# Kernel tuning notes

Measured on AMD Instinct MI355X. Metric: run time of the kernel, lower is better.

Reference implementation:

```python
import jax, jax.numpy as jnp
import numpy as np

B, S, HID = 1, 2048, 2048
H, KV, D = 16, 8, 128          # heads, kv heads, head_dim
EPS = 1e-6
THETA_T, THETA_HW = 1000000.0, 10000.0
SCALE = D ** -0.5
NEG = -1e9


def _rms(x, w):
    xf = x.astype(jnp.float32)
    var = jnp.mean(xf * xf, axis=-1, keepdims=True)
    return (w * (xf * jax.lax.rsqrt(var + EPS))).astype(x.dtype)


def _rope_cs(pos, theta, half_dim):
    # Module builds RoPE with head_dim = 2*half_dim then takes every-other freq:
    # exponents arange(0, 2*half_dim, 4) / (2*half_dim)  -> half_dim//2 freqs
    dim2 = 2 * half_dim
    inv_freq = 1.0 / theta ** (jnp.arange(0, dim2, 4, dtype=jnp.float32) / dim2)
    freqs = pos.astype(jnp.float32)[:, None] * inv_freq[None, :]   # [S, half_dim//2]
    emb = jnp.concatenate([freqs, freqs], axis=-1)                 # [S, half_dim]
    return jnp.cos(emb), jnp.sin(emb)


def _rot_half(x):
    d = x.shape[-1] // 2
    return jnp.concatenate([-x[..., d:], x[..., :d]], axis=-1)


def _apply_rope(q, k, cos, sin):
    cos = cos[None, None]  # [1,1,S,dim]
    sin = sin[None, None]
    return q * cos + _rot_half(q) * sin, k * cos + _rot_half(k) * sin


def setup_inputs() -> dict:
    key = jax.random.key(0)
    ks = jax.random.split(key, 10)
    hidden_states = jax.random.normal(ks[0], (B, S, HID), jnp.float32)
    indexes = jax.random.randint(ks[1], (3, S), 0, S)
    causal = jnp.tril(jnp.ones((S, S), bool))
    attention_mask = jnp.where(causal, 0.0, NEG).astype(jnp.float32)[None, None]
    qkv_w = jax.random.normal(ks[2], ((H + 2 * KV) * D, HID), jnp.float32) * 0.02
    qkv_b = jax.random.normal(ks[3], ((H + 2 * KV) * D,), jnp.float32) * 0.02
    o_w = jax.random.normal(ks[4], (HID, H * D), jnp.float32) * 0.02
    o_b = jax.random.normal(ks[5], (HID,), jnp.float32) * 0.02
    q_norm_w = jnp.ones((D // 2,), jnp.float32)
    k_norm_w = jnp.ones((D // 2,), jnp.float32)
    q_norm_hw_w = jnp.ones((D // 2,), jnp.float32)
    k_norm_hw_w = jnp.ones((D // 2,), jnp.float32)
    return dict(hidden_states=hidden_states, indexes=indexes, attention_mask=attention_mask,
                qkv_w=qkv_w, qkv_b=qkv_b, o_w=o_w, o_b=o_b,
                q_norm_w=q_norm_w, k_norm_w=k_norm_w,
                q_norm_hw_w=q_norm_hw_w, k_norm_hw_w=k_norm_hw_w)


def reference(hidden_states, indexes, attention_mask, qkv_w, qkv_b, o_w, o_b,
              q_norm_w, k_norm_w, q_norm_hw_w, k_norm_hw_w):
    b, s, _ = hidden_states.shape
    qkv = hidden_states @ qkv_w.T + qkv_b
    q, k, v = jnp.split(qkv, [H * D, H * D + KV * D], axis=-1)
    q = q.reshape(b, s, H, D)
    k = k.reshape(b, s, KV, D)
    v = v.reshape(b, s, KV, D)

    # split head_dim into time half and hw half
    q_t, q_hw = jnp.split(q, 2, axis=-1)
    k_t, k_hw = jnp.split(k, 2, axis=-1)
    q_t = jnp.swapaxes(_rms(q_t, q_norm_w), 1, 2)       # [B,H,S,D/2]
    k_t = jnp.swapaxes(_rms(k_t, k_norm_w), 1, 2)
    q_hw = jnp.swapaxes(_rms(q_hw, q_norm_hw_w), 1, 2)
    k_hw = jnp.swapaxes(_rms(k_hw, k_norm_hw_w), 1, 2)
    q_h, q_ww = jnp.split(q_hw, 2, axis=-1)             # [B,H,S,D/4]
    k_h, k_ww = jnp.split(k_hw, 2, axis=-1)

    cos_t, sin_t = _rope_cs(indexes[0], THETA_T, D // 2)
    q_t, k_t = _apply_rope(q_t, k_t, cos_t, sin_t)
    cos_h, sin_h = _rope_cs(indexes[1], THETA_HW, D // 4)
    q_h, k_h = _apply_rope(q_h, k_h, cos_h, sin_h)
    cos_w, sin_w = _rope_cs(indexes[2], THETA_HW, D // 4)
    q_ww, k_ww = _apply_rope(q_ww, k_ww, cos_w, sin_w)

    query = jnp.concatenate([q_t, q_h, q_ww], axis=-1)  # [B,H,S,D]
    keyst = jnp.concatenate([k_t, k_h, k_ww], axis=-1)  # [B,KV,S,D]
    value = jnp.swapaxes(v, 1, 2)                       # [B,KV,S,D]

    n_rep = H // KV
    keyst = jnp.repeat(keyst, n_rep, axis=1)
    value = jnp.repeat(value, n_rep, axis=1)

    scores = jnp.einsum('bhsd,bhtd->bhst', query, keyst) * SCALE + attention_mask
    probs = jax.nn.softmax(scores.astype(jnp.float32), axis=-1).astype(query.dtype)
    attn = jnp.einsum('bhst,bhtd->bhsd', probs, value)
    attn = jnp.swapaxes(attn, 1, 2).reshape(b, s, H * D)
    return attn @ o_w.T + o_b
```

## Files before the change

### kernel.cpp

```cpp
#include <hip/hip_runtime.h>

typedef __bf16 bf16;
typedef __bf16 bf16x4 __attribute__((ext_vector_type(4)));
typedef __bf16 bf16x8 __attribute__((ext_vector_type(8)));
typedef float f32x4 __attribute__((ext_vector_type(4)));

#define S_LEN 2048
#define HIDDEN 2048
#define NH 16
#define NKV 8
#define HD 128
#define QKV_N 4096

__device__ __forceinline__ void async_load16(const void* g, void* l) {
  __builtin_amdgcn_global_load_lds((const __attribute__((address_space(1))) unsigned int*)g,
                                   (__attribute__((address_space(3))) unsigned int*)l,
                                   16, 0, 0);
}

template <int C>
__device__ __forceinline__ float dpp_f(float x) {
  return __builtin_bit_cast(float, __builtin_amdgcn_mov_dpp(
      __builtin_bit_cast(int, x), C, 0xF, 0xF, true));
}
__device__ __forceinline__ float rowmax16(float x) {
  x = fmaxf(x, dpp_f<0x128>(x));
  x = fmaxf(x, dpp_f<0x124>(x));
  x = fmaxf(x, dpp_f<0x122>(x));
  x = fmaxf(x, dpp_f<0x121>(x));
  return x;
}
__device__ __forceinline__ float rowsum16(float x) {
  x += dpp_f<0x128>(x);
  x += dpp_f<0x124>(x);
  x += dpp_f<0x122>(x);
  x += dpp_f<0x121>(x);
  return x;
}

__global__ __launch_bounds__(256)
void cvt_f32_bf16(const float* __restrict__ src, bf16* __restrict__ dst, int n) {
  int i = (blockIdx.x * 256 + threadIdx.x) * 4;
  if (i < n) {
    float4 v = *(const float4*)(src + i);
    bf16x4 o = {(bf16)v.x, (bf16)v.y, (bf16)v.z, (bf16)v.w};
    *(bf16x4*)(dst + i) = o;
  }
}

template <int WRITE_BF16>
__global__ __launch_bounds__(256)
void gemm_bt(const bf16* __restrict__ A, const bf16* __restrict__ B,
             const float* __restrict__ bias, void* __restrict__ Cout,
             int M, int N, int K) {
  __shared__ bf16 As[2][128 * 32];
  __shared__ bf16 Bs[2][128 * 32];
  const int tid = threadIdx.x;
  const int w = tid >> 6, lane = tid & 63;
  const int quad = lane >> 4, l15 = lane & 15;
  const int wm = w >> 1, wn = w & 1;
  const int m0 = blockIdx.y * 128, n0 = blockIdx.x * 128;

  f32x4 acc[4][4];
#pragma unroll
  for (int i = 0; i < 4; i++)
#pragma unroll
    for (int j = 0; j < 4; j++) acc[i][j] = (f32x4){0.f, 0.f, 0.f, 0.f};

  const int crow = lane >> 2;
  const int ccol = (lane & 3) * 8;

#pragma unroll
  for (int q = 0; q < 2; q++) {
    int c = 2 * w + q;
    async_load16(A + (size_t)(m0 + c * 16 + crow) * K + ccol, (char*)As[0] + c * 1024);
    async_load16(B + (size_t)(n0 + c * 16 + crow) * K + ccol, (char*)Bs[0] + c * 1024);
  }

  int cur = 0;
  for (int k0 = 0; k0 < K; k0 += 32) {
    __asm__ __volatile__("s_waitcnt vmcnt(0)" ::: "memory");
    __syncthreads();
    if (k0 + 32 < K) {
#pragma unroll
      for (int q = 0; q < 2; q++) {
        int c = 2 * w + q;
        async_load16(A + (size_t)(m0 + c * 16 + crow) * K + k0 + 32 + ccol,
                     (char*)As[cur ^ 1] + c * 1024);
        async_load16(B + (size_t)(n0 + c * 16 + crow) * K + k0 + 32 + ccol,
                     (char*)Bs[cur ^ 1] + c * 1024);
      }
    }
    bf16x8 af[4], bfr[4];
#pragma unroll
    for (int i = 0; i < 4; i++)
      af[i] = *(const bf16x8*)(As[cur] + (wm * 64 + i * 16 + l15) * 32 + quad * 8);
#pragma unroll
    for (int j = 0; j < 4; j++)
      bfr[j] = *(const bf16x8*)(Bs[cur] + (wn * 64 + j * 16 + l15) * 32 + quad * 8);
#pragma unroll
    for (int i = 0; i < 4; i++)
#pragma unroll
      for (int j = 0; j < 4; j++)
        acc[i][j] = __builtin_amdgcn_mfma_f32_16x16x32_bf16(af[i], bfr[j], acc[i][j], 0, 0, 0);
    cur ^= 1;
  }

#pragma unroll
  for (int i = 0; i < 4; i++) {
#pragma unroll
    for (int j = 0; j < 4; j++) {
      int col = n0 + wn * 64 + j * 16 + l15;
      float bv = bias[col];
#pragma unroll
      for (int r = 0; r < 4; r++) {
        int row = m0 + wm * 64 + i * 16 + quad * 4 + r;
        float v = acc[i][j][r] + bv;
        if (WRITE_BF16)
          ((bf16*)Cout)[(size_t)row * N + col] = (bf16)v;
        else
          ((float*)Cout)[(size_t)row * N + col] = v;
      }
    }
  }
}

__global__ __launch_bounds__(128)
void normrope(const bf16* __restrict__ qkv, const int* __restrict__ idx,
              const float* __restrict__ qnw, const float* __restrict__ knw,
              const float* __restrict__ qnhw, const float* __restrict__ knhw,
              bf16* __restrict__ Qb, bf16* __restrict__ Kb) {
  const int s = blockIdx.x;
  const int y = blockIdx.y;
  const int d = threadIdx.x;

  const bool isq = (y < 16);
  const int off = isq ? (y * HD + d) : (2048 + (y - 16) * HD + d);
  float x = (float)qkv[(size_t)s * QKV_N + off];

  float ss = x * x;
#pragma unroll
  for (int o = 32; o; o >>= 1) ss += __shfl_xor(ss, o);
  float inv = rsqrtf(ss * (1.f / 64.f) + 1e-6f);
  const float* wt = (d < 64) ? (isq ? qnw : knw) : (isq ? qnhw : knhw);
  float yn = x * inv * wt[d & 63];

  float pos, invf;
  int xorm;
  bool firsthalf;
  if (d < 64) {
    pos = (float)idx[s];
    int i = d & 31;
    invf = exp2f(-(float)i * 0.6228615177913804f);
    xorm = 32;
    firsthalf = (d < 32);
  } else {
    int j = d - 64;
    int region = j >> 5;
    pos = (float)idx[(1 + region) * S_LEN + s];
    int i = j & 15;
    invf = exp2f(-(float)i * 0.8304820237218406f);
    xorm = 16;
    firsthalf = ((j & 31) < 16);
  }
  float ang = pos * invf;
  float si, co;
  sincosf(ang, &si, &co);
  float partner = __shfl_xor(yn, xorm);
  float outv = firsthalf ? (yn * co - partner * si) : (yn * co + partner * si);

  if (isq)
    Qb[((size_t)y * S_LEN + s) * HD + d] = (bf16)(outv * 0.12751745f);
  else
    Kb[((size_t)(y - 16) * S_LEN + s) * HD + d] = (bf16)outv;
}

__global__ __launch_bounds__(256)
void vtrans(const bf16* __restrict__ qkv, bf16* __restrict__ VT) {
  __shared__ bf16 T[64][72];
  const int tid = threadIdx.x;
  const int s0 = blockIdx.x * 64, d0 = blockIdx.y * 64, kv = blockIdx.z;
#pragma unroll
  for (int it = 0; it < 2; it++) {
    int r = (tid >> 3) + it * 32;
    int c = (tid & 7) * 8;
    bf16x8 v = *(const bf16x8*)(qkv + (size_t)(s0 + r) * QKV_N + 3072 + kv * HD + d0 + c);
    *(bf16x8*)(&T[r][c]) = v;
  }
  __syncthreads();
#pragma unroll
  for (int it = 0; it < 2; it++) {
    int r = (tid >> 3) + it * 32;
    int c = (tid & 7) * 8;
    bf16x8 o;
#pragma unroll
    for (int j = 0; j < 8; j++) o[j] = T[c + j][r];
    *(bf16x8*)(VT + ((size_t)kv * HD + d0 + r) * S_LEN + s0 + c) = o;
  }
}

__global__ __launch_bounds__(256)
void attn_fused(const bf16* __restrict__ Qb, const bf16* __restrict__ Kb,
                const bf16* __restrict__ VT, bf16* __restrict__ attnO,
                float* __restrict__ Opart, float* __restrict__ Ml) {
  __shared__ bf16 Kbuf[2][8192];
  __shared__ bf16 Vbuf[8192];
  __shared__ __align__(16) bf16 Ps[4][16][72];
  const int tid = threadIdx.x;
  const int w = tid >> 6, lane = tid & 63;
  const int quad = lane >> 4, l15 = lane & 15;
  const int b = blockIdx.x;
  const int h = b & 15;
  const int cid = b >> 4;
  int g, c;
  if (cid < 32) { g = 16 + (cid >> 1); c = cid & 1; }
  else          { g = cid - 32;        c = 0; }
  const int nT = g + 1;
  const int tBeg = c ? 16 : 0;
  const int tEnd = c ? nT : (nT < 16 ? nT : 16);
  const int qr0 = g * 64 + w * 16;
  const int kv = h >> 1;

  const bf16* Qg = Qb + (size_t)h * S_LEN * HD;
  const bf16* Kg = Kb + (size_t)kv * S_LEN * HD;
  const bf16* Vg = VT + (size_t)kv * HD * S_LEN;

  const bf16* ksrc = Kg + (size_t)(w * 16 + l15) * HD + quad * 8;
  const bf16* vsrc = Vg + (size_t)(2 * w * 16 + l15) * S_LEN + quad * 8;

  bf16x8 aq[4];
#pragma unroll
  for (int kc = 0; kc < 4; kc++)
    aq[kc] = *(const bf16x8*)(Qg + (size_t)(qr0 + l15) * HD + kc * 32 + quad * 8);

  float m2[4], li[4];
  f32x4 Oacc[8];
#pragma unroll
  for (int r = 0; r < 4; r++) { m2[r] = -1e30f; li[r] = 0.f; }
#pragma unroll
  for (int dt = 0; dt < 8; dt++) Oacc[dt] = (f32x4){0.f, 0.f, 0.f, 0.f};

#pragma unroll
  for (int kc = 0; kc < 4; kc++)
    async_load16(ksrc + (size_t)(tBeg << 6) * HD + kc * 32,
                 (char*)Kbuf[tBeg & 1] + (w * 4 + kc) * 1024);

  for (int tt = tBeg; tt < tEnd; ++tt) {
    const int t0 = tt << 6;
    const int cur = tt & 1;
    const bool more = (tt + 1 < tEnd);
    __asm__ __volatile__("s_waitcnt vmcnt(0)" ::: "memory");
    __syncthreads();

#pragma unroll
    for (int e = 0; e < 2; e++)
#pragma unroll
      for (int half = 0; half < 2; half++)
        async_load16(vsrc + (size_t)e * 16 * S_LEN + t0 + half * 32,
                     (char*)Vbuf + (half * 8 + 2 * w + e) * 1024);
    if (more) {
#pragma unroll
      for (int kc = 0; kc < 4; kc++)
        async_load16(ksrc + (size_t)(t0 + 64) * HD + kc * 32,
                     (char*)Kbuf[cur ^ 1] + (w * 4 + kc) * 1024);
    }

    f32x4 sacc[4];
#pragma unroll
    for (int nt = 0; nt < 4; nt++) {
      sacc[nt] = (f32x4){0.f, 0.f, 0.f, 0.f};
#pragma unroll
      for (int kc = 0; kc < 4; kc++) {
        bf16x8 bk = *(const bf16x8*)((const char*)Kbuf[cur] + (nt * 4 + kc) * 1024 + lane * 16);
        sacc[nt] = __builtin_amdgcn_mfma_f32_16x16x32_bf16(aq[kc], bk, sacc[nt], 0, 0, 0);
      }
    }

    const bool full = (t0 + 64 <= qr0);
    float mxv[4];
    bool need = false;
#pragma unroll
    for (int r = 0; r < 4; r++) {
      if (!full) {
        const int mrow = qr0 + quad * 4 + r;
        const int cb = t0 + l15;
        if (cb > mrow) sacc[0][r] = -1e30f;
        if (cb + 16 > mrow) sacc[1][r] = -1e30f;
        if (cb + 32 > mrow) sacc[2][r] = -1e30f;
        if (cb + 48 > mrow) sacc[3][r] = -1e30f;
      }
      mxv[r] = rowmax16(fmaxf(fmaxf(sacc[0][r], sacc[1][r]), fmaxf(sacc[2][r], sacc[3][r])));
      need = need || (mxv[r] > m2[r] + 8.f);
    }
    if (__any(need ? 1 : 0)) {
#pragma unroll
      for (int r = 0; r < 4; r++) {
        float mnew = fmaxf(m2[r], mxv[r]);
        float a = exp2f(m2[r] - mnew);
        li[r] *= a;
#pragma unroll
        for (int dt = 0; dt < 8; dt++) Oacc[dt][r] *= a;
        m2[r] = mnew;
      }
    }
#pragma unroll
    for (int r = 0; r < 4; r++) {
      float p0 = exp2f(sacc[0][r] - m2[r]);
      float p1 = exp2f(sacc[1][r] - m2[r]);
      float p2 = exp2f(sacc[2][r] - m2[r]);
      float p3 = exp2f(sacc[3][r] - m2[r]);
      li[r] += rowsum16((p0 + p1) + (p2 + p3));
      Ps[w][quad * 4 + r][l15] = (bf16)p0;
      Ps[w][quad * 4 + r][16 + l15] = (bf16)p1;
      Ps[w][quad * 4 + r][32 + l15] = (bf16)p2;
      Ps[w][quad * 4 + r][48 + l15] = (bf16)p3;
    }
    __asm__ __volatile__("s_waitcnt lgkmcnt(0)" ::: "memory");
    if (more)
      __asm__ __volatile__("s_waitcnt vmcnt(4)" ::: "memory");
    else
      __asm__ __volatile__("s_waitcnt vmcnt(0)" ::: "memory");

#pragma unroll
    for (int half = 0; half < 2; half++) {
      bf16x8 ap = *(const bf16x8*)(&Ps[w][l15][half * 32 + quad * 8]);
#pragma unroll
      for (int dt = 0; dt < 8; dt++) {
        bf16x8 bv = *(const bf16x8*)((const char*)Vbuf + (half * 8 + dt) * 1024 + lane * 16);
        Oacc[dt] = __builtin_amdgcn_mfma_f32_16x16x32_bf16(ap, bv, Oacc[dt], 0, 0, 0);
      }
    }
  }

  if (cid < 32) {
    float* Op = Opart + (size_t)b * 64 * 128;
    float* mlp = Ml + (size_t)b * 128;
#pragma unroll
    for (int r = 0; r < 4; r++) {
      const int row = w * 16 + quad * 4 + r;
#pragma unroll
      for (int dt = 0; dt < 8; dt++)
        Op[row * 128 + dt * 16 + l15] = Oacc[dt][r];
      if (l15 == 0) {
        mlp[row * 2 + 0] = m2[r];
        mlp[row * 2 + 1] = li[r];
      }
    }
  } else {
#pragma unroll
    for (int r = 0; r < 4; r++) {
      float invl = 1.f / li[r];
      int srow = qr0 + quad * 4 + r;
#pragma unroll
      for (int dt = 0; dt < 8; dt++)
        attnO[(size_t)srow * HIDDEN + h * HD + dt * 16 + l15] = (bf16)(Oacc[dt][r] * invl);
    }
  }
}

__global__ __launch_bounds__(256)
void attn_merge(const float* __restrict__ Opart, const float* __restrict__ Ml,
                bf16* __restrict__ attnO) {
  const int h = blockIdx.x & 15;
  const int g = 16 + (blockIdx.x >> 4);
  const int cid0 = (g - 16) * 2;
  const int bA = cid0 * 16 + h, bB = (cid0 + 1) * 16 + h;
  const float* OA = Opart + (size_t)bA * 64 * 128;
  const float* OB = Opart + (size_t)bB * 64 * 128;
  const float* mlA = Ml + (size_t)bA * 128;
  const float* mlB = Ml + (size_t)bB * 128;
  const int t = threadIdx.x;
#pragma unroll
  for (int it = 0; it < 8; ++it) {
    int e = it * 256 + t;
    int row = e >> 5, d = (e & 31) * 4;
    float mA = mlA[row * 2], lA = mlA[row * 2 + 1];
    float mB = mlB[row * 2], lB = mlB[row * 2 + 1];
    float m = fmaxf(mA, mB);
    float aA = exp2f(mA - m), aB = exp2f(mB - m);
    float inv = 1.f / (lA * aA + lB * aB);
    f32x4 a = *(const f32x4*)(OA + row * 128 + d);
    f32x4 bq = *(const f32x4*)(OB + row * 128 + d);
    int srow = g * 64 + row;
    bf16x4 o;
#pragma unroll
    for (int j = 0; j < 4; j++) o[j] = (bf16)((a[j] * aA + bq[j] * aB) * inv);
    *(bf16x4*)(attnO + (size_t)srow * HIDDEN + h * HD + d) = o;
  }
}

extern "C" void kernel_launch(void* const* d_in, const int* in_sizes, int n_in,
                              void* d_out, int out_size, void* d_ws, size_t ws_size,
                              hipStream_t stream) {
  const float* hidden = (const float*)d_in[0];
  const int* idx = (const int*)d_in[1];
  const float* qkv_w = (const float*)d_in[3];
  const float* qkv_b = (const float*)d_in[4];
  const float* o_w = (const float*)d_in[5];
  const float* o_b = (const float*)d_in[6];
  const float* qnw = (const float*)d_in[7];
  const float* knw = (const float*)d_in[8];
  const float* qnhw = (const float*)d_in[9];
  const float* knhw = (const float*)d_in[10];

  char* ws = (char*)d_ws;
  bf16* hB    = (bf16*)(ws);
  bf16* qwB   = (bf16*)(ws + (8u << 20));
  bf16* qkvB  = (bf16*)(ws + (24u << 20));
  bf16* Qb    = (bf16*)(ws + (40u << 20));
  bf16* Kb    = (bf16*)(ws + (48u << 20));
  bf16* VT    = (bf16*)(ws + (52u << 20));
  bf16* owB   = hB;
  float* Opart = (float*)(ws + (8u << 20));
  bf16* attn  = (bf16*)(ws + (24u << 20));
  float* Ml   = (float*)(ws + (32u << 20));

  cvt_f32_bf16<<<HIDDEN * S_LEN / 1024, 256, 0, stream>>>(hidden, hB, HIDDEN * S_LEN);
  cvt_f32_bf16<<<QKV_N * HIDDEN / 1024, 256, 0, stream>>>(qkv_w, qwB, QKV_N * HIDDEN);

  gemm_bt<1><<<dim3(QKV_N / 128, S_LEN / 128), 256, 0, stream>>>(
      hB, qwB, qkv_b, qkvB, S_LEN, QKV_N, HIDDEN);

  cvt_f32_bf16<<<HIDDEN * HIDDEN / 1024, 256, 0, stream>>>(o_w, owB, HIDDEN * HIDDEN);

  normrope<<<dim3(S_LEN, 24), 128, 0, stream>>>(qkvB, idx, qnw, knw, qnhw, knhw, Qb, Kb);
  vtrans<<<dim3(S_LEN / 64, HD / 64, NKV), 256, 0, stream>>>(qkvB, VT);

  attn_fused<<<768, 256, 0, stream>>>(Qb, Kb, VT, attn, Opart, Ml);
  attn_merge<<<256, 256, 0, stream>>>(Opart, Ml, attn);

  gemm_bt<0><<<dim3(HIDDEN / 128, S_LEN / 128), 256, 0, stream>>>(
      attn, owB, o_b, (float*)d_out, S_LEN, HIDDEN, HIDDEN);
}
```

Measured before the change: 316.4 us.

## Process two query tiles per attention block, rebalance KV splits, swizzle GEMM tiles

The attention kernel now has each block handle 128 query rows as two 64-row sub-tiles that share every K/V tile loaded into shared memory, which halves K/V global traffic per query row. The causal work is split into 1, 2 or 3 KV chunks of 14 tiles depending on row group, and the merge kernel now combines up to three partials. GEMM block indices are remapped so that each XCD works on its own contiguous set of output columns, for better L2 reuse. The two input f32-to-bf16 conversions are merged into one launch. In exchange the attention kernel holds more registers (two sets of Q fragments and accumulators), which may lower occupancy, and the workspace layout changes.

```diff
diff --git a/kernel.cpp b/kernel.cpp
--- a/kernel.cpp
+++ b/kernel.cpp
@@ -12,6 +12,8 @@
 #define HD 128
 #define QKV_N 4096
 
+#define PSLOT 66560
+
 __device__ __forceinline__ void async_load16(const void* g, void* l) {
   __builtin_amdgcn_global_load_lds((const __attribute__((address_space(1))) unsigned int*)g,
                                    (__attribute__((address_space(3))) unsigned int*)l,
@@ -46,6 +48,20 @@
     bf16x4 o = {(bf16)v.x, (bf16)v.y, (bf16)v.z, (bf16)v.w};
     *(bf16x4*)(dst + i) = o;
   }
+}
+
+__global__ __launch_bounds__(256)
+void cvt_pair(const float* __restrict__ s1, bf16* __restrict__ d1, int n1,
+              const float* __restrict__ s2, bf16* __restrict__ d2, int n2) {
+  int i = (blockIdx.x * 256 + threadIdx.x) * 4;
+  const float* s;
+  bf16* d;
+  int j;
+  if (i < n1) { s = s1; d = d1; j = i; }
+  else        { s = s2; d = d2; j = i - n1; if (j >= n2) return; }
+  float4 v = *(const float4*)(s + j);
+  bf16x4 o = {(bf16)v.x, (bf16)v.y, (bf16)v.z, (bf16)v.w};
+  *(bf16x4*)(d + j) = o;
 }
 
 template <int WRITE_BF16>
@@ -59,7 +75,13 @@
   const int w = tid >> 6, lane = tid & 63;
   const int quad = lane >> 4, l15 = lane & 15;
   const int wm = w >> 1, wn = w & 1;
-  const int m0 = blockIdx.y * 128, n0 = blockIdx.x * 128;
+
+  const int flat = blockIdx.y * gridDim.x + blockIdx.x;
+  const int xcd = flat & 7, loc = flat >> 3;
+  const int colsPer = gridDim.x >> 3;
+  const int nidx = xcd * colsPer + loc / gridDim.y;
+  const int midx = loc % gridDim.y;
+  const int m0 = midx * 128, n0 = nidx * 128;
 
   f32x4 acc[4][4];
 #pragma unroll
@@ -202,24 +224,26 @@
 __global__ __launch_bounds__(256)
 void attn_fused(const bf16* __restrict__ Qb, const bf16* __restrict__ Kb,
                 const bf16* __restrict__ VT, bf16* __restrict__ attnO,
-                float* __restrict__ Opart, float* __restrict__ Ml) {
+                char* __restrict__ Opart) {
   __shared__ bf16 Kbuf[2][8192];
   __shared__ bf16 Vbuf[8192];
-  __shared__ __align__(16) bf16 Ps[4][16][72];
+  __shared__ __align__(16) bf16 Ps[4][2][16][72];
   const int tid = threadIdx.x;
   const int w = tid >> 6, lane = tid & 63;
   const int quad = lane >> 4, l15 = lane & 15;
   const int b = blockIdx.x;
   const int h = b & 15;
   const int cid = b >> 4;
-  int g, c;
-  if (cid < 32) { g = 16 + (cid >> 1); c = cid & 1; }
-  else          { g = cid - 32;        c = 0; }
-  const int nT = g + 1;
-  const int tBeg = c ? 16 : 0;
-  const int tEnd = c ? nT : (nT < 16 ? nT : 16);
-  const int qr0 = g * 64 + w * 16;
+  int G, c, nc;
+  if (cid < 7)       { G = cid;          c = 0;     nc = 1; }
+  else if (cid < 21) { int t = cid - 7;  G = 7 + (t >> 1);  c = t & 1; nc = 2; }
+  else               { int t = cid - 21; G = 14 + t / 3;    c = t % 3; nc = 3; }
+  const int nT = 2 * G + 2;
+  const int tBeg = c * 14;
+  const int tEnd = (tBeg + 14 < nT) ? (tBeg + 14) : nT;
+  const int tCap0 = 2 * G + 1;
   const int kv = h >> 1;
+  const int qr0h[2] = {G * 128 + w * 16, G * 128 + 64 + w * 16};
 
   const bf16* Qg = Qb + (size_t)h * S_LEN * HD;
   const bf16* Kg = Kb + (size_t)kv * S_LEN * HD;
@@ -228,17 +252,22 @@
   const bf16* ksrc = Kg + (size_t)(w * 16 + l15) * HD + quad * 8;
   const bf16* vsrc = Vg + (size_t)(2 * w * 16 + l15) * S_LEN + quad * 8;
 
-  bf16x8 aq[4];
-#pragma unroll
-  for (int kc = 0; kc < 4; kc++)
-    aq[kc] = *(const bf16x8*)(Qg + (size_t)(qr0 + l15) * HD + kc * 32 + quad * 8);
-
-  float m2[4], li[4];
-  f32x4 Oacc[8];
-#pragma unroll
-  for (int r = 0; r < 4; r++) { m2[r] = -1e30f; li[r] = 0.f; }
-#pragma unroll
-  for (int dt = 0; dt < 8; dt++) Oacc[dt] = (f32x4){0.f, 0.f, 0.f, 0.f};
+  bf16x8 aq[2][4];
+#pragma unroll
+  for (int bb = 0; bb < 2; bb++)
+#pragma unroll
+    for (int kc = 0; kc < 4; kc++)
+      aq[bb][kc] = *(const bf16x8*)(Qg + (size_t)(qr0h[bb] + l15) * HD + kc * 32 + quad * 8);
+
+  float m2[2][4], li[2][4];
+  f32x4 Oacc[2][8];
+#pragma unroll
+  for (int bb = 0; bb < 2; bb++) {
+#pragma unroll
+    for (int r = 0; r < 4; r++) { m2[bb][r] = -1e30f; li[bb][r] = 0.f; }
+#pragma unroll
+    for (int dt = 0; dt < 8; dt++) Oacc[bb][dt] = (f32x4){0.f, 0.f, 0.f, 0.f};
+  }
 
 #pragma unroll
   for (int kc = 0; kc < 4; kc++)
@@ -249,6 +278,7 @@
     const int t0 = tt << 6;
     const int cur = tt & 1;
     const bool more = (tt + 1 < tEnd);
+    const bool do0 = (tt < tCap0);
     __asm__ __volatile__("s_waitcnt vmcnt(0)" ::: "memory");
     __syncthreads();
 
@@ -265,55 +295,59 @@
                      (char*)Kbuf[cur ^ 1] + (w * 4 + kc) * 1024);
     }
 
-    f32x4 sacc[4];
-#pragma unroll
-    for (int nt = 0; nt < 4; nt++) {
-      sacc[nt] = (f32x4){0.f, 0.f, 0.f, 0.f};
-#pragma unroll
-      for (int kc = 0; kc < 4; kc++) {
-        bf16x8 bk = *(const bf16x8*)((const char*)Kbuf[cur] + (nt * 4 + kc) * 1024 + lane * 16);
-        sacc[nt] = __builtin_amdgcn_mfma_f32_16x16x32_bf16(aq[kc], bk, sacc[nt], 0, 0, 0);
-      }
-    }
-
-    const bool full = (t0 + 64 <= qr0);
-    float mxv[4];
-    bool need = false;
-#pragma unroll
-    for (int r = 0; r < 4; r++) {
-      if (!full) {
-        const int mrow = qr0 + quad * 4 + r;
-        const int cb = t0 + l15;
-        if (cb > mrow) sacc[0][r] = -1e30f;
-        if (cb + 16 > mrow) sacc[1][r] = -1e30f;
-        if (cb + 32 > mrow) sacc[2][r] = -1e30f;
-        if (cb + 48 > mrow) sacc[3][r] = -1e30f;
-      }
-      mxv[r] = rowmax16(fmaxf(fmaxf(sacc[0][r], sacc[1][r]), fmaxf(sacc[2][r], sacc[3][r])));
-      need = need || (mxv[r] > m2[r] + 8.f);
-    }
-    if (__any(need ? 1 : 0)) {
+#pragma unroll
+    for (int bb = 0; bb < 2; bb++) {
+      if (bb == 0 && !do0) continue;
+      const int qr0 = qr0h[bb];
+      f32x4 sacc[4];
+#pragma unroll
+      for (int nt = 0; nt < 4; nt++) {
+        sacc[nt] = (f32x4){0.f, 0.f, 0.f, 0.f};
+#pragma unroll
+        for (int kc = 0; kc < 4; kc++) {
+          bf16x8 bk = *(const bf16x8*)((const char*)Kbuf[cur] + (nt * 4 + kc) * 1024 + lane * 16);
+          sacc[nt] = __builtin_amdgcn_mfma_f32_16x16x32_bf16(aq[bb][kc], bk, sacc[nt], 0, 0, 0);
+        }
+      }
+      const bool full = (t0 + 64 <= qr0);
+      float mxv[4];
+      bool need = false;
 #pragma unroll
       for (int r = 0; r < 4; r++) {
-        float mnew = fmaxf(m2[r], mxv[r]);
-        float a = exp2f(m2[r] - mnew);
-        li[r] *= a;
-#pragma unroll
-        for (int dt = 0; dt < 8; dt++) Oacc[dt][r] *= a;
-        m2[r] = mnew;
-      }
-    }
-#pragma unroll
-    for (int r = 0; r < 4; r++) {
-      float p0 = exp2f(sacc[0][r] - m2[r]);
-      float p1 = exp2f(sacc[1][r] - m2[r]);
-      float p2 = exp2f(sacc[2][r] - m2[r]);
-      float p3 = exp2f(sacc[3][r] - m2[r]);
-      li[r] += rowsum16((p0 + p1) + (p2 + p3));
-      Ps[w][quad * 4 + r][l15] = (bf16)p0;
-      Ps[w][quad * 4 + r][16 + l15] = (bf16)p1;
-      Ps[w][quad * 4 + r][32 + l15] = (bf16)p2;
-      Ps[w][quad * 4 + r][48 + l15] = (bf16)p3;
+        if (!full) {
+          const int mrow = qr0 + quad * 4 + r;
+          const int cb = t0 + l15;
+          if (cb > mrow) sacc[0][r] = -1e30f;
+          if (cb + 16 > mrow) sacc[1][r] = -1e30f;
+          if (cb + 32 > mrow) sacc[2][r] = -1e30f;
+          if (cb + 48 > mrow) sacc[3][r] = -1e30f;
+        }
+        mxv[r] = rowmax16(fmaxf(fmaxf(sacc[0][r], sacc[1][r]), fmaxf(sacc[2][r], sacc[3][r])));
+        need = need || (mxv[r] > m2[bb][r] + 8.f);
+      }
+      if (__any(need ? 1 : 0)) {
+#pragma unroll
+        for (int r = 0; r < 4; r++) {
+          float mnew = fmaxf(m2[bb][r], mxv[r]);
+          float a = exp2f(m2[bb][r] - mnew);
+          li[bb][r] *= a;
+#pragma unroll
+          for (int dt = 0; dt < 8; dt++) Oacc[bb][dt][r] *= a;
+          m2[bb][r] = mnew;
+        }
+      }
+#pragma unroll
+      for (int r = 0; r < 4; r++) {
+        float p0 = exp2f(sacc[0][r] - m2[bb][r]);
+        float p1 = exp2f(sacc[1][r] - m2[bb][r]);
+        float p2 = exp2f(sacc[2][r] - m2[bb][r]);
+        float p3 = exp2f(sacc[3][r] - m2[bb][r]);
+        li[bb][r] += rowsum16((p0 + p1) + (p2 + p3));
+        Ps[w][bb][quad * 4 + r][l15] = (bf16)p0;
+        Ps[w][bb][quad * 4 + r][16 + l15] = (bf16)p1;
+        Ps[w][bb][quad * 4 + r][32 + l15] = (bf16)p2;
+        Ps[w][bb][quad * 4 + r][48 + l15] = (bf16)p3;
+      }
     }
     __asm__ __volatile__("s_waitcnt lgkmcnt(0)" ::: "memory");
     if (more)
@@ -322,69 +356,90 @@
       __asm__ __volatile__("s_waitcnt vmcnt(0)" ::: "memory");
 
 #pragma unroll
-    for (int half = 0; half < 2; half++) {
-      bf16x8 ap = *(const bf16x8*)(&Ps[w][l15][half * 32 + quad * 8]);
-#pragma unroll
-      for (int dt = 0; dt < 8; dt++) {
-        bf16x8 bv = *(const bf16x8*)((const char*)Vbuf + (half * 8 + dt) * 1024 + lane * 16);
-        Oacc[dt] = __builtin_amdgcn_mfma_f32_16x16x32_bf16(ap, bv, Oacc[dt], 0, 0, 0);
-      }
-    }
-  }
-
-  if (cid < 32) {
-    float* Op = Opart + (size_t)b * 64 * 128;
-    float* mlp = Ml + (size_t)b * 128;
-#pragma unroll
-    for (int r = 0; r < 4; r++) {
-      const int row = w * 16 + quad * 4 + r;
-#pragma unroll
-      for (int dt = 0; dt < 8; dt++)
-        Op[row * 128 + dt * 16 + l15] = Oacc[dt][r];
-      if (l15 == 0) {
-        mlp[row * 2 + 0] = m2[r];
-        mlp[row * 2 + 1] = li[r];
+    for (int bb = 0; bb < 2; bb++) {
+      if (bb == 0 && !do0) continue;
+#pragma unroll
+      for (int half = 0; half < 2; half++) {
+        bf16x8 ap = *(const bf16x8*)(&Ps[w][bb][l15][half * 32 + quad * 8]);
+#pragma unroll
+        for (int dt = 0; dt < 8; dt++) {
+          bf16x8 bv = *(const bf16x8*)((const char*)Vbuf + (half * 8 + dt) * 1024 + lane * 16);
+          Oacc[bb][dt] = __builtin_amdgcn_mfma_f32_16x16x32_bf16(ap, bv, Oacc[bb][dt], 0, 0, 0);
+        }
+      }
+    }
+  }
+
+  if (nc > 1) {
+    char* slot = Opart + (size_t)((cid - 7) * 16 + h) * PSLOT;
+    float* Op = (float*)slot;
+    float* mlp = (float*)(slot + 65536);
+#pragma unroll
+    for (int bb = 0; bb < 2; bb++) {
+#pragma unroll
+      for (int r = 0; r < 4; r++) {
+        const int row = bb * 64 + w * 16 + quad * 4 + r;
+#pragma unroll
+        for (int dt = 0; dt < 8; dt++)
+          Op[row * 128 + dt * 16 + l15] = Oacc[bb][dt][r];
+        if (l15 == 0) {
+          mlp[row * 2 + 0] = m2[bb][r];
+          mlp[row * 2 + 1] = li[bb][r];
+        }
       }
     }
   } else {
 #pragma unroll
-    for (int r = 0; r < 4; r++) {
-      float invl = 1.f / li[r];
-      int srow = qr0 + quad * 4 + r;
-#pragma unroll
-      for (int dt = 0; dt < 8; dt++)
-        attnO[(size_t)srow * HIDDEN + h * HD + dt * 16 + l15] = (bf16)(Oacc[dt][r] * invl);
-    }
-  }
-}
-
-__global__ __launch_bounds__(256)
-void attn_merge(const float* __restrict__ Opart, const float* __restrict__ Ml,
-                bf16* __restrict__ attnO) {
+    for (int bb = 0; bb < 2; bb++) {
+#pragma unroll
+      for (int r = 0; r < 4; r++) {
+        float invl = 1.f / li[bb][r];
+        int srow = qr0h[bb] + quad * 4 + r;
+#pragma unroll
+        for (int dt = 0; dt < 8; dt++)
+          attnO[(size_t)srow * HIDDEN + h * HD + dt * 16 + l15] = (bf16)(Oacc[bb][dt][r] * invl);
+      }
+    }
+  }
+}
+
+__global__ __launch_bounds__(256)
+void attn_merge(const char* __restrict__ Opart, bf16* __restrict__ attnO) {
   const int h = blockIdx.x & 15;
-  const int g = 16 + (blockIdx.x >> 4);
-  const int cid0 = (g - 16) * 2;
-  const int bA = cid0 * 16 + h, bB = (cid0 + 1) * 16 + h;
-  const float* OA = Opart + (size_t)bA * 64 * 128;
-  const float* OB = Opart + (size_t)bB * 64 * 128;
-  const float* mlA = Ml + (size_t)bA * 128;
-  const float* mlB = Ml + (size_t)bB * 128;
+  const int idx = blockIdx.x >> 4;
+  int G, nc, cid0;
+  if (idx < 7) { G = 7 + idx;        nc = 2; cid0 = 7 + idx * 2; }
+  else         { G = 14 + (idx - 7); nc = 3; cid0 = 21 + (idx - 7) * 3; }
+  const char* s0 = Opart + (size_t)((cid0 - 7) * 16 + h) * PSLOT;
+  const char* s1 = s0 + (size_t)16 * PSLOT;
+  const char* s2 = s0 + (size_t)32 * PSLOT;
+  const float* O0 = (const float*)s0;
+  const float* O1 = (const float*)s1;
+  const float* O2 = (const float*)s2;
+  const float* ML0 = (const float*)(s0 + 65536);
+  const float* ML1 = (const float*)(s1 + 65536);
+  const float* ML2 = (const float*)(s2 + 65536);
   const int t = threadIdx.x;
 #pragma unroll
-  for (int it = 0; it < 8; ++it) {
+  for (int it = 0; it < 16; ++it) {
     int e = it * 256 + t;
     int row = e >> 5, d = (e & 31) * 4;
-    float mA = mlA[row * 2], lA = mlA[row * 2 + 1];
-    float mB = mlB[row * 2], lB = mlB[row * 2 + 1];
-    float m = fmaxf(mA, mB);
-    float aA = exp2f(mA - m), aB = exp2f(mB - m);
-    float inv = 1.f / (lA * aA + lB * aB);
-    f32x4 a = *(const f32x4*)(OA + row * 128 + d);
-    f32x4 bq = *(const f32x4*)(OB + row * 128 + d);
-    int srow = g * 64 + row;
+    float m0 = ML0[row * 2], l0 = ML0[row * 2 + 1];
+    float m1 = ML1[row * 2], l1 = ML1[row * 2 + 1];
+    float m2v = -1e30f, l2v = 0.f;
+    if (nc == 3) { m2v = ML2[row * 2]; l2v = ML2[row * 2 + 1]; }
+    float m = fmaxf(fmaxf(m0, m1), m2v);
+    float a0 = exp2f(m0 - m), a1 = exp2f(m1 - m), a2 = exp2f(m2v - m);
+    float inv = 1.f / (a0 * l0 + a1 * l1 + a2 * l2v);
+    f32x4 x0 = *(const f32x4*)(O0 + row * 128 + d);
+    f32x4 x1 = *(const f32x4*)(O1 + row * 128 + d);
+    f32x4 x2 = (f32x4){0.f, 0.f, 0.f, 0.f};
+    if (nc == 3) x2 = *(const f32x4*)(O2 + row * 128 + d);
+    int srow = G * 128 + row;
     bf16x4 o;
 #pragma unroll
-    for (int j = 0; j < 4; j++) o[j] = (bf16)((a[j] * aA + bq[j] * aB) * inv);
+    for (int j = 0; j < 4; j++)
+      o[j] = (bf16)((a0 * x0[j] + a1 * x1[j] + a2 * x2[j]) * inv);
     *(bf16x4*)(attnO + (size_t)srow * HIDDEN + h * HD + d) = o;
   }
 }
@@ -411,12 +466,11 @@
   bf16* Kb    = (bf16*)(ws + (48u << 20));
   bf16* VT    = (bf16*)(ws + (52u << 20));
   bf16* owB   = hB;
-  float* Opart = (float*)(ws + (8u << 20));
-  bf16* attn  = (bf16*)(ws + (24u << 20));
-  float* Ml   = (float*)(ws + (32u << 20));
-
-  cvt_f32_bf16<<<HIDDEN * S_LEN / 1024, 256, 0, stream>>>(hidden, hB, HIDDEN * S_LEN);
-  cvt_f32_bf16<<<QKV_N * HIDDEN / 1024, 256, 0, stream>>>(qkv_w, qwB, QKV_N * HIDDEN);
+  char* Opart = ws + (8u << 20);
+  bf16* attn  = (bf16*)(ws + (32u << 20));
+
+  cvt_pair<<<12288, 256, 0, stream>>>(hidden, hB, HIDDEN * S_LEN,
+                                      qkv_w, qwB, QKV_N * HIDDEN);
 
   gemm_bt<1><<<dim3(QKV_N / 128, S_LEN / 128), 256, 0, stream>>>(
       hB, qwB, qkv_b, qkvB, S_LEN, QKV_N, HIDDEN);
@@ -426,8 +480,8 @@
   normrope<<<dim3(S_LEN, 24), 128, 0, stream>>>(qkvB, idx, qnw, knw, qnhw, knhw, Qb, Kb);
   vtrans<<<dim3(S_LEN / 64, HD / 64, NKV), 256, 0, stream>>>(qkvB, VT);
 
-  attn_fused<<<768, 256, 0, stream>>>(Qb, Kb, VT, attn, Opart, Ml);
-  attn_merge<<<256, 256, 0, stream>>>(Opart, Ml, attn);
+  attn_fused<<<432, 256, 0, stream>>>(Qb, Kb, VT, attn, Opart);
+  attn_merge<<<144, 256, 0, stream>>>(Opart, attn);
 
   gemm_bt<0><<<dim3(HIDDEN / 128, S_LEN / 128), 256, 0, stream>>>(
       attn, owB, o_b, (float*)d_out, S_LEN, HIDDEN, HIDDEN);
```

Measured after the change: 317.0 us. Within noise of the previous version (+0.2%).
